# Performance work log

Measured on AMD Instinct MI355X. Metric: run time of the kernel, lower is better.

## Reference

```python
import math
import jax, jax.numpy as jnp
import numpy as np

# ---- static config ----
B, S, HID = 2, 8192, 1024
H, D = 8, 128                      # num_heads, head_dim = hidden // heads
CHUNK = 128                        # attention_chunk_size
PAST = 128 - 1                     # attention_context_left - 1
FUT = 128                          # attention_context_right
CTX = CHUNK + PAST + FUT           # 383
POS = CTX + 1                      # relative position table length (rel_shift pads to CTX+1)
CAP = 50.0                         # attention_logit_cap
Q_SCALE = D ** (-0.5) / math.log(2.0)
K_SCALE = math.log1p(math.e) / math.log(2.0)
NB = S // CHUNK                    # 64 blocks (S divisible by chunk -> no tail padding)


def setup_inputs() -> dict:
    key = jax.random.key(0)
    ks = jax.random.split(key, 8)
    s = 0.02
    return {
        "hidden_states": jax.random.normal(ks[0], (B, S, HID), jnp.float32),
        "position_embeddings": jax.random.normal(ks[1], (POS, HID), jnp.float32),
        "Wq": jax.random.normal(ks[2], (HID, H * D), jnp.float32) * s,
        "Wk": jax.random.normal(ks[3], (HID, H * D), jnp.float32) * s,
        "Wv": jax.random.normal(ks[4], (HID, H * D), jnp.float32) * s,
        "Wrel": jax.random.normal(ks[5], (HID, H * D), jnp.float32) * s,
        "Wpost": jax.random.normal(ks[6], (HID, HID), jnp.float32) * s,
        "per_dim_scale": jax.random.normal(ks[7], (D,), jnp.float32) * 0.1,
    }


def reference(hidden_states, position_embeddings, Wq, Wk, Wv, Wrel, Wpost, per_dim_scale):
    # projections (clipped-linear clamps are +/-inf -> no-ops); bias-free linears
    q = (hidden_states @ Wq).reshape(B, S, H, D)
    k = (hidden_states @ Wk).reshape(B, S, H, D)
    v = (hidden_states @ Wv).reshape(B, S, H, D)

    q = q * (Q_SCALE * jax.nn.softplus(per_dim_scale))  # per-dim scaling fused into q
    k = k * K_SCALE

    # _convert_to_block: [B, NB, CHUNK, H, D] (S % CHUNK == 0 -> no pad)
    qb = q.reshape(B, NB, CHUNK, H, D)

    # _extract_block_context: pad (PAST, FUT + CHUNK - 1) then unfold window=CTX step=CHUNK
    pad = ((0, 0), (PAST, FUT + CHUNK - 1), (0, 0), (0, 0))
    kp = jnp.pad(k, pad)
    vp = jnp.pad(v, pad)
    idx = jnp.arange(NB)[:, None] * CHUNK + jnp.arange(CTX)[None, :]  # [NB, CTX]
    kc = kp[:, idx]  # [B, NB, CTX, H, D]
    vc = vp[:, idx]  # [B, NB, CTX, H, D]

    # relative keys: [POS, H, D]
    rel_k = (position_embeddings @ Wrel).reshape(POS, H, D)

    # content scores: [B, H, NB, CHUNK, CTX]
    ac = jnp.einsum('bnchd,bnkhd->bhnck', qb, kc)
    # position scores before shift: [B, H, NB, CHUNK, POS]
    bd = jnp.einsum('bnchd,phd->bhncp', qb, rel_k)
    # Transformer-XL rel_shift (POS == CTX+1 so pad amount is zero)
    bd = bd.reshape(B, H, NB, CHUNK * POS)[..., : CHUNK * CTX]
    bd = bd.reshape(B, H, NB, CHUNK, CTX)

    # tanh soft-cap + softmax (no attention_mask)
    logits = jnp.tanh((ac + bd) / CAP) * CAP
    attn = jax.nn.softmax(logits, axis=-1)

    # weighted values -> [B, NB, CHUNK, H, D] -> [B, S, HID]
    out = jnp.einsum('bhnck,bnkhd->bnchd', attn, vc).reshape(B, S, H * D)
    return out @ Wpost
```

## Files before the change

### kernel.cpp

```cpp
#include <hip/hip_runtime.h>
#include <cmath>


using bf16x8 = __attribute__((ext_vector_type(8))) short;
using f32x4  = __attribute__((ext_vector_type(4))) float;
using s16x4  = __attribute__((ext_vector_type(4))) short;

__device__ __forceinline__ short f2bf(float f) {
  unsigned u = __float_as_uint(f);
  u = (u + 0x7FFF + ((u >> 16) & 1)) >> 16;
  return (short)u;
}
__device__ __forceinline__ float bf2f(unsigned short s) {
  return __uint_as_float(((unsigned)s) << 16);
}

__device__ __forceinline__ void gl16(void* lds, const void* gptr) {
  __builtin_amdgcn_global_load_lds(
      (const __attribute__((address_space(1))) unsigned int*)gptr,
      (__attribute__((address_space(3))) unsigned int*)lds, 16, 0, 0);
}

__global__ void cvt_bf16_k(const float* __restrict__ in, short* __restrict__ out, int n) {
  int i = (blockIdx.x * 256 + threadIdx.x) * 4;
  if (i + 3 < n) {
    float4 v = *(const float4*)&in[i];
    s16x4 o;
    o[0] = f2bf(v.x); o[1] = f2bf(v.y); o[2] = f2bf(v.z); o[3] = f2bf(v.w);
    *(s16x4*)&out[i] = o;
  }
}

__global__ void wtrans_k(const float* __restrict__ W, short* __restrict__ Wt) {
  __shared__ float T[64 * 65];
  const int tid = threadIdx.x;
  const int bx = blockIdx.x, by = blockIdx.y;
#pragma unroll
  for (int it = 0; it < 4; ++it) {
    int ci = it * 256 + tid;
    int k = ci >> 4, n4 = (ci & 15) * 4;
    float4 v = *(const float4*)&W[(size_t)(by * 64 + k) * 1024 + bx * 64 + n4];
    T[k * 65 + n4 + 0] = v.x;
    T[k * 65 + n4 + 1] = v.y;
    T[k * 65 + n4 + 2] = v.z;
    T[k * 65 + n4 + 3] = v.w;
  }
  __syncthreads();
#pragma unroll
  for (int it = 0; it < 2; ++it) {
    int co = it * 256 + tid;
    int nn = co >> 3, k8 = (co & 7) * 8;
    bf16x8 o;
#pragma unroll
    for (int jj = 0; jj < 8; ++jj) o[jj] = f2bf(T[(k8 + jj) * 65 + nn]);
    *(bf16x8*)&Wt[(size_t)(bx * 64 + nn) * 1024 + by * 64 + k8] = o;
  }
}

__global__ void qscale_k(const float* __restrict__ pds, float* __restrict__ qs, double qsb) {
  int d = threadIdx.x;
  double x = (double)pds[d];
  qs[d] = (float)(qsb * log1p(exp(x)));
}

__global__ void vpadzero_k(short* __restrict__ vpadT) {
  int row = blockIdx.x;
  int t = threadIdx.x;
  int key = (t < 127) ? t : (8192 + t);
  vpadT[(size_t)row * 8448 + key] = 0;
}


__device__ __forceinline__ void stage_half(short* ldsb, const short* gbase, int tid) {
#pragma unroll
  for (int it = 0; it < 2; ++it) {
    int L = (it * 512 + tid) * 16;
    int r = L >> 7;
    int cb = (L & 127) ^ (((L >> 9) & 1) << 5);
    gl16((char*)ldsb + L, gbase + (size_t)r * 1024 + (cb >> 1));
  }
}

__device__ __forceinline__ bf16x8 frag_ld(const short* hb, int row, int ks, int q4) {
  int cb = (ks * 64 + q4 * 16) ^ (((row >> 2) & 1) << 5);
  return *(const bf16x8*)((const char*)hb + row * 128 + cb);
}

__global__ __launch_bounds__(512, 2)
void qkv256_k(const short* __restrict__ A, const short* __restrict__ Bt3,
              short* __restrict__ q_bf, short* __restrict__ kpad,
              short* __restrict__ vpadT,
              const float* __restrict__ qsc, float kscale) {
  __shared__ __align__(16) short lds[65536];

  const int tid = threadIdx.x;
  const int lane = tid & 63, wid = tid >> 6;
  const int q4 = lane >> 4, l16 = lane & 15;
  const int wr = wid >> 2, wc = wid & 3;

  const int id = blockIdx.x;
  const int xcd = id & 7, local = id >> 3;
  const int mm = xcd * 8 + local / 12, nn = local % 12;
  const int m0 = mm * 256, n0 = nn * 256;

  const short* Abase = A + (size_t)m0 * 1024;
  const short* Bbase = Bt3 + (size_t)n0 * 1024;

  const f32x4 z4 = {0.f, 0.f, 0.f, 0.f};
  f32x4 acc[8][4];
#pragma unroll
  for (int i = 0; i < 8; ++i)
#pragma unroll
    for (int j = 0; j < 4; ++j) acc[i][j] = z4;

  stage_half(lds + 0 * 32768 + 0 * 8192, Abase, tid);
  stage_half(lds + 0 * 32768 + 1 * 8192, Abase + 128 * 1024, tid);
  stage_half(lds + 0 * 32768 + 2 * 8192, Bbase, tid);
  stage_half(lds + 0 * 32768 + 3 * 8192, Bbase + 128 * 1024, tid);
  stage_half(lds + 1 * 32768 + 2 * 8192, Bbase + 64, tid);
  stage_half(lds + 1 * 32768 + 3 * 8192, Bbase + 128 * 1024 + 64, tid);
  asm volatile("s_waitcnt vmcnt(4)" ::: "memory");
  __builtin_amdgcn_s_barrier();

  for (int kt = 0; kt < 16; ++kt) {
    const int buf = kt & 1;
    const short* Acur = lds + buf * 32768 + wr * 8192;
    const short* Bcur = lds + buf * 32768 + (2 + (wc >> 1)) * 8192;
    const int brow0 = (wc & 1) * 64;

    bf16x8 bfr[4][2];

    {
#pragma unroll
      for (int j = 0; j < 4; ++j)
#pragma unroll
        for (int ks = 0; ks < 2; ++ks)
          bfr[j][ks] = frag_ld(Bcur, brow0 + j * 16 + l16, ks, q4);
      bf16x8 afr[2][2];
#pragma unroll
      for (int m2 = 0; m2 < 2; ++m2)
#pragma unroll
        for (int ks = 0; ks < 2; ++ks)
          afr[m2][ks] = frag_ld(Acur, m2 * 16 + l16, ks, q4);
      if (kt < 15)
        stage_half(lds + (buf ^ 1) * 32768 + 0 * 8192, Abase + (size_t)(kt + 1) * 64, tid);
      asm volatile("s_waitcnt lgkmcnt(8)" ::: "memory");
      __builtin_amdgcn_s_barrier();
      asm volatile("s_waitcnt lgkmcnt(0)" ::: "memory");
      __builtin_amdgcn_s_setprio(1);
#pragma unroll
      for (int ks = 0; ks < 2; ++ks)
#pragma unroll
        for (int m2 = 0; m2 < 2; ++m2)
#pragma unroll
          for (int j = 0; j < 4; ++j)
            acc[m2][j] = __builtin_amdgcn_mfma_f32_16x16x32_bf16(
                afr[m2][ks], bfr[j][ks], acc[m2][j], 0, 0, 0);
      __builtin_amdgcn_s_setprio(0);
      __builtin_amdgcn_s_barrier();
    }

#pragma unroll
    for (int p = 1; p < 4; ++p) {
      bf16x8 afr[2][2];
#pragma unroll
      for (int m2 = 0; m2 < 2; ++m2)
#pragma unroll
        for (int ks = 0; ks < 2; ++ks)
          afr[m2][ks] = frag_ld(Acur, (p * 2 + m2) * 16 + l16, ks, q4);
      if (p == 1) {
        if (kt < 15)
          stage_half(lds + (buf ^ 1) * 32768 + 1 * 8192,
                     Abase + 128 * 1024 + (size_t)(kt + 1) * 64, tid);
      } else if (p == 2) {
        if (kt < 14)
          stage_half(lds + buf * 32768 + 2 * 8192, Bbase + (size_t)(kt + 2) * 64, tid);
      } else {
        if (kt < 14)
          stage_half(lds + buf * 32768 + 3 * 8192,
                     Bbase + 128 * 1024 + (size_t)(kt + 2) * 64, tid);
      }
      __builtin_amdgcn_s_barrier();
      asm volatile("s_waitcnt lgkmcnt(0)" ::: "memory");
      __builtin_amdgcn_s_setprio(1);
#pragma unroll
      for (int ks = 0; ks < 2; ++ks)
#pragma unroll
        for (int m2 = 0; m2 < 2; ++m2)
#pragma unroll
          for (int j = 0; j < 4; ++j)
            acc[p * 2 + m2][j] = __builtin_amdgcn_mfma_f32_16x16x32_bf16(
                afr[m2][ks], bfr[j][ks], acc[p * 2 + m2][j], 0, 0, 0);
      __builtin_amdgcn_s_setprio(0);
      if (p == 3) {
        if (kt < 14) asm volatile("s_waitcnt vmcnt(4)" ::: "memory");
        else         asm volatile("s_waitcnt vmcnt(0)" ::: "memory");
      }
      __builtin_amdgcn_s_barrier();
    }
  }

  const int w = n0 >> 10;
  const int cw = n0 & 1023;
  const int b = m0 >> 13;
  const int s_base = (m0 & 8191) + wr * 128;

  if (w == 0) {
    float qsv[4];
#pragma unroll
    for (int j = 0; j < 4; ++j) qsv[j] = qsc[(cw + wc * 64 + j * 16 + l16) & 127];
#pragma unroll
    for (int m = 0; m < 8; ++m)
#pragma unroll
      for (int j = 0; j < 4; ++j)
#pragma unroll
        for (int rg = 0; rg < 4; ++rg) {
          int s = s_base + m * 16 + q4 * 4 + rg;
          int col = cw + wc * 64 + j * 16 + l16;
          int h = col >> 7, d = col & 127;
          int n = s >> 7, c = s & 127;
          q_bf[((size_t)(((b * 64 + n) * 8 + h) * 128 + c)) * 128 + d] =
              f2bf(acc[m][j][rg] * qsv[j]);
        }
  } else if (w == 1) {
#pragma unroll
    for (int m = 0; m < 8; ++m)
#pragma unroll
      for (int j = 0; j < 4; ++j)
#pragma unroll
        for (int rg = 0; rg < 4; ++rg) {
          int s = s_base + m * 16 + q4 * 4 + rg;
          int col = cw + wc * 64 + j * 16 + l16;
          int h = col >> 7, d = col & 127;
          kpad[((size_t)(b * 8 + h) * 8448 + 127 + s) * 128 + d] =
              f2bf(acc[m][j][rg] * kscale);
        }
  } else {
    short* T = lds;
#pragma unroll
    for (int hh = 0; hh < 2; ++hh) {
      __syncthreads();
      if ((wc >> 1) == hh) {
#pragma unroll
        for (int m = 0; m < 8; ++m)
#pragma unroll
          for (int j = 0; j < 4; ++j)
#pragma unroll
            for (int rg = 0; rg < 4; ++rg) {
              int sl = wr * 128 + m * 16 + q4 * 4 + rg;
              int dl = (wc & 1) * 64 + j * 16 + l16;
              T[dl * 264 + sl] = f2bf(acc[m][j][rg]);
            }
      }
      __syncthreads();
      const int h = (cw >> 7) + hh;
#pragma unroll
      for (int it = 0; it < 8; ++it) {
        int co = it * 512 + tid;
        int dd = co >> 5, s8 = (co & 31) * 8;
        *(bf16x8*)&vpadT[((size_t)(b * 8 + h) * 128 + dd) * 8448 + 127 + (m0 & 8191) + s8] =
            *(const bf16x8*)&T[dd * 264 + s8];
      }
    }
  }
}

__global__ __launch_bounds__(256, 3)
void post_gemm_k(const short* __restrict__ A, const short* __restrict__ Bt,
                 float* __restrict__ outf) {
  __shared__ __align__(16) short As[128 * 32];
  __shared__ __align__(16) short Bs[128 * 32];

  const int tid = threadIdx.x;
  const int lane = tid & 63, wid = tid >> 6;
  const int q4 = lane >> 4, l16 = lane & 15;
  const int wr = wid >> 1, wc = wid & 1;

  const int id = blockIdx.x;
  const int xcd = id & 7, local = id >> 3;
  const int mm = local >> 3, nn = local & 7;
  const int m0 = (xcd * 16 + mm) * 128, n0 = nn * 128;

  const f32x4 z4 = {0.f, 0.f, 0.f, 0.f};
  f32x4 acc[4][4];
#pragma unroll
  for (int i = 0; i < 4; ++i)
#pragma unroll
    for (int j = 0; j < 4; ++j) acc[i][j] = z4;

  const int r0 = tid >> 2, s0_ = (tid & 3) * 8;

  for (int kk = 0; kk < 1024; kk += 32) {
    __syncthreads();
    gl16(&As[tid * 8],         A  + (size_t)(m0 + r0) * 1024 + kk + s0_);
    gl16(&Bs[tid * 8],         Bt + (size_t)(n0 + r0) * 1024 + kk + s0_);
    gl16(&As[(256 + tid) * 8], A  + (size_t)(m0 + 64 + r0) * 1024 + kk + s0_);
    gl16(&Bs[(256 + tid) * 8], Bt + (size_t)(n0 + 64 + r0) * 1024 + kk + s0_);
    __syncthreads();
    bf16x8 af[4], bfv[4];
#pragma unroll
    for (int i = 0; i < 4; ++i)
      af[i] = *(const bf16x8*)&As[(wr * 64 + i * 16 + l16) * 32 + q4 * 8];
#pragma unroll
    for (int j = 0; j < 4; ++j)
      bfv[j] = *(const bf16x8*)&Bs[(wc * 64 + j * 16 + l16) * 32 + q4 * 8];
#pragma unroll
    for (int i = 0; i < 4; ++i)
#pragma unroll
      for (int j = 0; j < 4; ++j)
        acc[i][j] = __builtin_amdgcn_mfma_f32_16x16x32_bf16(af[i], bfv[j], acc[i][j], 0, 0, 0);
  }

#pragma unroll
  for (int i = 0; i < 4; ++i)
#pragma unroll
    for (int j = 0; j < 4; ++j)
#pragma unroll
      for (int rg = 0; rg < 4; ++rg) {
        const int row = m0 + wr * 64 + i * 16 + q4 * 4 + rg;
        const int col = n0 + wc * 64 + j * 16 + l16;
        outf[(size_t)row * 1024 + col] = acc[i][j][rg];
      }
}

__global__ __launch_bounds__(256, 2)
void rel_gemm_k(const short* __restrict__ A, const short* __restrict__ Bt,
                short* __restrict__ relk) {
  __shared__ __align__(16) short As[128 * 32];
  __shared__ __align__(16) short Bs[128 * 32];

  const int tid = threadIdx.x;
  const int lane = tid & 63, wid = tid >> 6;
  const int q4 = lane >> 4, l16 = lane & 15;
  const int wr = wid >> 1, wc = wid & 1;
  const int m0 = blockIdx.x * 128, n0 = blockIdx.y * 128;

  const f32x4 z4 = {0.f, 0.f, 0.f, 0.f};
  f32x4 acc[4][4];
#pragma unroll
  for (int i = 0; i < 4; ++i)
#pragma unroll
    for (int j = 0; j < 4; ++j) acc[i][j] = z4;

  const int r0 = tid >> 2, s0_ = (tid & 3) * 8;
  for (int kk = 0; kk < 1024; kk += 32) {
    __syncthreads();
    gl16(&As[tid * 8],         A  + (size_t)(m0 + r0) * 1024 + kk + s0_);
    gl16(&Bs[tid * 8],         Bt + (size_t)(n0 + r0) * 1024 + kk + s0_);
    gl16(&As[(256 + tid) * 8], A  + (size_t)(m0 + 64 + r0) * 1024 + kk + s0_);
    gl16(&Bs[(256 + tid) * 8], Bt + (size_t)(n0 + 64 + r0) * 1024 + kk + s0_);
    __syncthreads();
    bf16x8 af[4], bfv[4];
#pragma unroll
    for (int i = 0; i < 4; ++i)
      af[i] = *(const bf16x8*)&As[(wr * 64 + i * 16 + l16) * 32 + q4 * 8];
#pragma unroll
    for (int j = 0; j < 4; ++j)
      bfv[j] = *(const bf16x8*)&Bs[(wc * 64 + j * 16 + l16) * 32 + q4 * 8];
#pragma unroll
    for (int i = 0; i < 4; ++i)
#pragma unroll
      for (int j = 0; j < 4; ++j)
        acc[i][j] = __builtin_amdgcn_mfma_f32_16x16x32_bf16(af[i], bfv[j], acc[i][j], 0, 0, 0);
  }

#pragma unroll
  for (int i = 0; i < 4; ++i)
#pragma unroll
    for (int j = 0; j < 4; ++j)
#pragma unroll
      for (int rg = 0; rg < 4; ++rg) {
        const int row = m0 + wr * 64 + i * 16 + q4 * 4 + rg;
        const int col = n0 + wc * 64 + j * 16 + l16;
        int h = col >> 7, d = col & 127;
        relk[(size_t)(h * 384 + row) * 128 + d] = f2bf(acc[i][j][rg]);
      }
}

__global__ __launch_bounds__(256, 2)
void bd_gemm_k(const short* __restrict__ qb_b, const short* __restrict__ relk,
               short* __restrict__ bds) {
  __shared__ __align__(16) short As[128 * 32];
  __shared__ __align__(16) short Bs[128 * 32];
  const int tid = threadIdx.x;
  const int lane = tid & 63, wid = tid >> 6;
  const int q4 = lane >> 4, l16 = lane & 15;
  const int wr = wid >> 1, wc = wid & 1;
  const int p0 = blockIdx.x * 128;
  const int nh = blockIdx.y;
  const int h = nh & 7;
  const short* A = qb_b + (size_t)nh * 16384;
  const short* Bt = relk + (size_t)h * (384 * 128);
  short* bdo = bds + (size_t)nh * 49152;

  const f32x4 z4 = {0.f, 0.f, 0.f, 0.f};
  f32x4 acc[4][4];
#pragma unroll
  for (int i = 0; i < 4; ++i)
#pragma unroll
    for (int j = 0; j < 4; ++j) acc[i][j] = z4;

  const int r0 = tid >> 2, s0_ = (tid & 3) * 8;
  for (int kk = 0; kk < 128; kk += 32) {
    __syncthreads();
    gl16(&As[tid * 8],         A  + (size_t)r0 * 128 + kk + s0_);
    gl16(&Bs[tid * 8],         Bt + (size_t)(p0 + r0) * 128 + kk + s0_);
    gl16(&As[(256 + tid) * 8], A  + (size_t)(64 + r0) * 128 + kk + s0_);
    gl16(&Bs[(256 + tid) * 8], Bt + (size_t)(p0 + 64 + r0) * 128 + kk + s0_);
    __syncthreads();
    bf16x8 af[4], bfv[4];
#pragma unroll
    for (int i = 0; i < 4; ++i)
      af[i] = *(const bf16x8*)&As[(wr * 64 + i * 16 + l16) * 32 + q4 * 8];
#pragma unroll
    for (int j = 0; j < 4; ++j)
      bfv[j] = *(const bf16x8*)&Bs[(wc * 64 + j * 16 + l16) * 32 + q4 * 8];
#pragma unroll
    for (int i = 0; i < 4; ++i)
#pragma unroll
      for (int j = 0; j < 4; ++j)
        acc[i][j] = __builtin_amdgcn_mfma_f32_16x16x32_bf16(af[i], bfv[j], acc[i][j], 0, 0, 0);
  }

#pragma unroll
  for (int i = 0; i < 4; ++i)
#pragma unroll
    for (int j = 0; j < 4; ++j)
#pragma unroll
      for (int rg = 0; rg < 4; ++rg) {
        int r = wr * 64 + i * 16 + q4 * 4 + rg;
        int p = p0 + wc * 64 + j * 16 + l16;
        int t = r + p;
        int c = (t < 383) ? r : (r + 1);
        int k = (t < 383) ? t : (t - 383);
        if (c < 128) {
          int tt = k >> 7, jj = (k >> 4) & 7, ll = k & 15;
          int wa = c >> 5, ia = (c >> 4) & 1, qa = (c >> 2) & 3, ra = c & 3;
          bdo[((((size_t)tt * 8 + jj) * 256) + wa * 64 + qa * 16 + ll) * 8 + ia * 4 + ra] =
              f2bf(acc[i][j][rg]);
        }
      }
}

__global__ __launch_bounds__(256, 3)
void attn_k(const short* __restrict__ qb_b, const short* __restrict__ kpad,
            const short* __restrict__ vpadT, const short* __restrict__ bds,
            short* __restrict__ attnout, int b) {
  __shared__ __align__(16) short Ks[4 * 128 * 32];
  __shared__ __align__(16) short Ps[64 * 136];

  const int tid = threadIdx.x;
  const int lane = tid & 63, wid = tid >> 6;
  const int q4 = lane >> 4, l16 = lane & 15;
  const int bx = blockIdx.x;
  const int qh = bx & 1, nh = bx >> 1;
  const int n = nh >> 3, h = nh & 7;

  const short* qtile = qb_b + (size_t)nh * 16384 + qh * 64 * 128;
  const short* kbase = kpad + ((size_t)(b * 8 + h) * 8448 + n * 128) * 128;
  const short* vtb = vpadT + (size_t)(b * 8 + h) * 128 * 8448 + n * 128;
  const short* bdb = bds + (size_t)nh * 49152;

#pragma unroll
  for (int it = 0; it < 4; ++it) {
    int ci = it * 256 + tid;
    int dc = ci >> 8, rr = (ci >> 2) & 63, sub = (ci & 3) * 8;
    gl16(&Ks[ci * 8], qtile + rr * 128 + dc * 32 + sub);
  }
  __syncthreads();
  bf16x8 qf[4];
#pragma unroll
  for (int dc = 0; dc < 4; ++dc)
    qf[dc] = *(const bf16x8*)&Ks[dc * 2048 + (wid * 16 + l16) * 32 + q4 * 8];

  const f32x4 z4 = {0.f, 0.f, 0.f, 0.f};
  f32x4 acco[8];
#pragma unroll
  for (int j = 0; j < 8; ++j) acco[j] = z4;
  float rsum[4] = {};

  for (int t = 0; t < 3; ++t) {
    __syncthreads();
#pragma unroll
    for (int it = 0; it < 8; ++it) {
      int ci = it * 256 + tid;
      int dc = ci >> 9, rr = (ci >> 2) & 127, sub = (ci & 3) * 8;
      gl16(&Ks[ci * 8], kbase + (size_t)(t * 128 + rr) * 128 + dc * 32 + sub);
    }

    s16x4 bdv[8];
#pragma unroll
    for (int j = 0; j < 8; ++j)
      bdv[j] = *(const s16x4*)&bdb[((((size_t)t * 8 + j) * 256) +
                 (qh * 2 + (wid >> 1)) * 64 + q4 * 16 + l16) * 8 + (wid & 1) * 4];

    __syncthreads();

    f32x4 accs[8];
#pragma unroll
    for (int j = 0; j < 8; ++j) accs[j] = z4;
#pragma unroll
    for (int dc = 0; dc < 4; ++dc) {
      bf16x8 kf[8];
#pragma unroll
      for (int j = 0; j < 8; ++j)
        kf[j] = *(const bf16x8*)&Ks[dc * 4096 + (j * 16 + l16) * 32 + q4 * 8];
#pragma unroll
      for (int j = 0; j < 8; ++j)
        accs[j] = __builtin_amdgcn_mfma_f32_16x16x32_bf16(qf[dc], kf[j], accs[j], 0, 0, 0);
    }

#pragma unroll
    for (int j = 0; j < 8; ++j) {
      const int kg = t * 128 + j * 16 + l16;
#pragma unroll
      for (int rg = 0; rg < 4; ++rg) {
        float sv = accs[j][rg] + bf2f((unsigned short)bdv[j][rg]);
        float tt = exp2f(sv * 0.057707801635558534f);
        float wgt = exp2f(-144.26950408889634f * __fdividef(1.0f, tt + 1.0f));
        wgt = (kg < 383) ? wgt : 0.0f;
        accs[j][rg] = wgt;
        rsum[rg] += wgt;
      }
    }
    __syncthreads();

#pragma unroll
    for (int it = 0; it < 8; ++it) {
      int ci = it * 256 + tid;
      int kc = ci >> 9, dd = (ci >> 2) & 127, sub = (ci & 3) * 8;
      gl16(&Ks[ci * 8], vtb + (size_t)dd * 8448 + t * 128 + kc * 32 + sub);
    }
#pragma unroll
    for (int j = 0; j < 8; ++j)
#pragma unroll
      for (int rg = 0; rg < 4; ++rg) {
        int c = wid * 16 + q4 * 4 + rg;
        int kl = j * 16 + l16;
        Ps[c * 136 + kl] = f2bf(accs[j][rg]);
      }
    __syncthreads();

#pragma unroll
    for (int kc = 0; kc < 4; ++kc) {
      bf16x8 pf, vf[8];
      pf = *(const bf16x8*)&Ps[(wid * 16 + l16) * 136 + kc * 32 + q4 * 8];
#pragma unroll
      for (int j = 0; j < 8; ++j)
        vf[j] = *(const bf16x8*)&Ks[kc * 4096 + (j * 16 + l16) * 32 + q4 * 8];
#pragma unroll
      for (int j = 0; j < 8; ++j)
        acco[j] = __builtin_amdgcn_mfma_f32_16x16x32_bf16(pf, vf[j], acco[j], 0, 0, 0);
    }
  }

  float rinv[4];
#pragma unroll
  for (int rg = 0; rg < 4; ++rg) {
    float rs = rsum[rg];
    rs += __shfl_xor(rs, 1);
    rs += __shfl_xor(rs, 2);
    rs += __shfl_xor(rs, 4);
    rs += __shfl_xor(rs, 8);
    rinv[rg] = __fdividef(1.0f, rs);
  }
#pragma unroll
  for (int j = 0; j < 8; ++j)
#pragma unroll
    for (int rg = 0; rg < 4; ++rg) {
      int srow = n * 128 + qh * 64 + wid * 16 + q4 * 4 + rg;
      int col = h * 128 + j * 16 + l16;
      attnout[((size_t)b * 8192 + srow) * 1024 + col] = f2bf(acco[j][rg] * rinv[rg]);
    }
}

extern "C" void kernel_launch(void* const* d_in, const int* in_sizes, int n_in,
                              void* d_out, int out_size, void* d_ws, size_t ws_size,
                              hipStream_t stream) {
  (void)in_sizes; (void)n_in; (void)out_size; (void)ws_size;
  const float* hs    = (const float*)d_in[0];
  const float* pemb  = (const float*)d_in[1];
  const float* Wq    = (const float*)d_in[2];
  const float* Wk    = (const float*)d_in[3];
  const float* Wv    = (const float*)d_in[4];
  const float* Wrel  = (const float*)d_in[5];
  const float* Wpost = (const float*)d_in[6];
  const float* pds   = (const float*)d_in[7];
  float* out = (float*)d_out;

  char* w = (char*)d_ws;
  auto alloc = [&](size_t bytes) -> char* {
    char* p = w; w += (bytes + 255) & ~(size_t)255; return p;
  };
  short* hs_bf   = (short*)alloc((size_t)16384 * 1024 * 2);
  short* pos_bf  = (short*)alloc((size_t)384 * 1024 * 2);
  short* Wq_t    = (short*)alloc((size_t)1024 * 1024 * 2);
  short* Wk_t    = (short*)alloc((size_t)1024 * 1024 * 2);
  short* Wv_t    = (short*)alloc((size_t)1024 * 1024 * 2);
  short* Wrel_t  = (short*)alloc((size_t)1024 * 1024 * 2);
  short* Wpost_t = (short*)alloc((size_t)1024 * 1024 * 2);
  float* qsc     = (float*)alloc(512);
  short* q_bf    = (short*)alloc((size_t)2 * 64 * 8 * 128 * 128 * 2);
  short* kpad    = (short*)alloc((size_t)2 * 8 * 8448 * 128 * 2);
  short* vpadT   = (short*)alloc((size_t)2 * 8 * 128 * 8448 * 2);
  short* relk    = (short*)alloc((size_t)8 * 384 * 128 * 2);
  short* bds     = (short*)alloc((size_t)64 * 8 * 128 * 384 * 2);
  short* attnout = hs_bf;

  const float kscale = (float)(log1p(exp(1.0)) / log(2.0));
  const double qsb = (1.0 / sqrt(128.0)) / log(2.0);

  cvt_bf16_k<<<16384, 256, 0, stream>>>(hs, hs_bf, 16384 * 1024);
  cvt_bf16_k<<<384, 256, 0, stream>>>(pemb, pos_bf, 384 * 1024);
  dim3 tg(16, 16);
  wtrans_k<<<tg, 256, 0, stream>>>(Wq, Wq_t);
  wtrans_k<<<tg, 256, 0, stream>>>(Wk, Wk_t);
  wtrans_k<<<tg, 256, 0, stream>>>(Wv, Wv_t);
  wtrans_k<<<tg, 256, 0, stream>>>(Wrel, Wrel_t);
  wtrans_k<<<tg, 256, 0, stream>>>(Wpost, Wpost_t);
  qscale_k<<<1, 128, 0, stream>>>(pds, qsc, qsb);
  hipMemsetAsync(kpad, 0, (size_t)2 * 8 * 8448 * 128 * 2, stream);
  vpadzero_k<<<2048, 256, 0, stream>>>(vpadT);

  qkv256_k<<<768, 512, 0, stream>>>(hs_bf, Wq_t, q_bf, kpad, vpadT, qsc, kscale);
  rel_gemm_k<<<dim3(3, 8), 256, 0, stream>>>(pos_bf, Wrel_t, relk);

  for (int b = 0; b < 2; ++b) {
    const short* qb_b = q_bf + (size_t)b * 64 * 8 * 128 * 128;
    bd_gemm_k<<<dim3(3, 512), 256, 0, stream>>>(qb_b, relk, bds);
    attn_k<<<1024, 256, 0, stream>>>(qb_b, kpad, vpadT, bds, attnout, b);
  }

  post_gemm_k<<<1024, 256, 0, stream>>>(attnout, Wpost_t, out);
}
```

Measured before the change: 544.2 us.

## Replace post-projection GEMM with 256x256 double-buffered pipelined kernel and XOR swizzle

The output projection GEMM moves from 128x128 tiles with a single 32-wide K stage to 256x256 tiles with 512 threads, 64-wide K steps, double-buffered LDS, staggered async global-to-LDS loads and MFMA priority hints. This is the same scheme the QKV kernel uses. The LDS swizzle is changed to a full 8-slot XOR pattern that both the QKV and post kernels share, to reduce bank conflicts. It cuts per-tile load overhead and barrier stalls, but launches only 256 blocks and relies on hand-placed waitcnt and barriers being correct.

```diff
diff --git a/kernel.cpp b/kernel.cpp
--- a/kernel.cpp
+++ b/kernel.cpp
@@ -74,16 +74,17 @@
 __device__ __forceinline__ void stage_half(short* ldsb, const short* gbase, int tid) {
 #pragma unroll
   for (int it = 0; it < 2; ++it) {
-    int L = (it * 512 + tid) * 16;
-    int r = L >> 7;
-    int cb = (L & 127) ^ (((L >> 9) & 1) << 5);
-    gl16((char*)ldsb + L, gbase + (size_t)r * 1024 + (cb >> 1));
+    int idx = it * 512 + tid;
+    int r = idx >> 3;
+    int slot = idx & 7;
+    int src = (slot ^ (r & 7)) << 3;
+    gl16((char*)ldsb + idx * 16, gbase + (size_t)r * 1024 + src);
   }
 }
 
 __device__ __forceinline__ bf16x8 frag_ld(const short* hb, int row, int ks, int q4) {
-  int cb = (ks * 64 + q4 * 16) ^ (((row >> 2) & 1) << 5);
-  return *(const bf16x8*)((const char*)hb + row * 128 + cb);
+  int slot = (ks * 4 + q4) ^ (row & 7);
+  return *(const bf16x8*)((const char*)hb + row * 128 + slot * 16);
 }
 
 __global__ __launch_bounds__(512, 2)
@@ -265,61 +266,127 @@
   }
 }
 
-__global__ __launch_bounds__(256, 3)
-void post_gemm_k(const short* __restrict__ A, const short* __restrict__ Bt,
-                 float* __restrict__ outf) {
-  __shared__ __align__(16) short As[128 * 32];
-  __shared__ __align__(16) short Bs[128 * 32];
+__global__ __launch_bounds__(512, 2)
+void post256_k(const short* __restrict__ A, const short* __restrict__ Bt,
+               float* __restrict__ outf) {
+  __shared__ __align__(16) short lds[65536];
 
   const int tid = threadIdx.x;
   const int lane = tid & 63, wid = tid >> 6;
   const int q4 = lane >> 4, l16 = lane & 15;
-  const int wr = wid >> 1, wc = wid & 1;
+  const int wr = wid >> 2, wc = wid & 3;
 
   const int id = blockIdx.x;
   const int xcd = id & 7, local = id >> 3;
-  const int mm = local >> 3, nn = local & 7;
-  const int m0 = (xcd * 16 + mm) * 128, n0 = nn * 128;
+  const int mm = xcd * 8 + (local >> 2), nn = local & 3;
+  const int m0 = mm * 256, n0 = nn * 256;
+
+  const short* Abase = A + (size_t)m0 * 1024;
+  const short* Bbase = Bt + (size_t)n0 * 1024;
 
   const f32x4 z4 = {0.f, 0.f, 0.f, 0.f};
-  f32x4 acc[4][4];
-#pragma unroll
-  for (int i = 0; i < 4; ++i)
+  f32x4 acc[8][4];
+#pragma unroll
+  for (int i = 0; i < 8; ++i)
 #pragma unroll
     for (int j = 0; j < 4; ++j) acc[i][j] = z4;
 
-  const int r0 = tid >> 2, s0_ = (tid & 3) * 8;
-
-  for (int kk = 0; kk < 1024; kk += 32) {
-    __syncthreads();
-    gl16(&As[tid * 8],         A  + (size_t)(m0 + r0) * 1024 + kk + s0_);
-    gl16(&Bs[tid * 8],         Bt + (size_t)(n0 + r0) * 1024 + kk + s0_);
-    gl16(&As[(256 + tid) * 8], A  + (size_t)(m0 + 64 + r0) * 1024 + kk + s0_);
-    gl16(&Bs[(256 + tid) * 8], Bt + (size_t)(n0 + 64 + r0) * 1024 + kk + s0_);
-    __syncthreads();
-    bf16x8 af[4], bfv[4];
-#pragma unroll
-    for (int i = 0; i < 4; ++i)
-      af[i] = *(const bf16x8*)&As[(wr * 64 + i * 16 + l16) * 32 + q4 * 8];
+  stage_half(lds + 0 * 32768 + 0 * 8192, Abase, tid);
+  stage_half(lds + 0 * 32768 + 1 * 8192, Abase + 128 * 1024, tid);
+  stage_half(lds + 0 * 32768 + 2 * 8192, Bbase, tid);
+  stage_half(lds + 0 * 32768 + 3 * 8192, Bbase + 128 * 1024, tid);
+  stage_half(lds + 1 * 32768 + 2 * 8192, Bbase + 64, tid);
+  stage_half(lds + 1 * 32768 + 3 * 8192, Bbase + 128 * 1024 + 64, tid);
+  asm volatile("s_waitcnt vmcnt(4)" ::: "memory");
+  __builtin_amdgcn_s_barrier();
+
+  for (int kt = 0; kt < 16; ++kt) {
+    const int buf = kt & 1;
+    const short* Acur = lds + buf * 32768 + wr * 8192;
+    const short* Bcur = lds + buf * 32768 + (2 + (wc >> 1)) * 8192;
+    const int brow0 = (wc & 1) * 64;
+
+    bf16x8 bfr[4][2];
+
+    {
+#pragma unroll
+      for (int j = 0; j < 4; ++j)
+#pragma unroll
+        for (int ks = 0; ks < 2; ++ks)
+          bfr[j][ks] = frag_ld(Bcur, brow0 + j * 16 + l16, ks, q4);
+      bf16x8 afr[2][2];
+#pragma unroll
+      for (int m2 = 0; m2 < 2; ++m2)
+#pragma unroll
+        for (int ks = 0; ks < 2; ++ks)
+          afr[m2][ks] = frag_ld(Acur, m2 * 16 + l16, ks, q4);
+      if (kt < 15)
+        stage_half(lds + (buf ^ 1) * 32768 + 0 * 8192, Abase + (size_t)(kt + 1) * 64, tid);
+      asm volatile("s_waitcnt lgkmcnt(8)" ::: "memory");
+      __builtin_amdgcn_s_barrier();
+      asm volatile("s_waitcnt lgkmcnt(0)" ::: "memory");
+      __builtin_amdgcn_s_setprio(1);
+#pragma unroll
+      for (int ks = 0; ks < 2; ++ks)
+#pragma unroll
+        for (int m2 = 0; m2 < 2; ++m2)
+#pragma unroll
+          for (int j = 0; j < 4; ++j)
+            acc[m2][j] = __builtin_amdgcn_mfma_f32_16x16x32_bf16(
+                afr[m2][ks], bfr[j][ks], acc[m2][j], 0, 0, 0);
+      __builtin_amdgcn_s_setprio(0);
+      __builtin_amdgcn_s_barrier();
+    }
+
+#pragma unroll
+    for (int p = 1; p < 4; ++p) {
+      bf16x8 afr[2][2];
+#pragma unroll
+      for (int m2 = 0; m2 < 2; ++m2)
+#pragma unroll
+        for (int ks = 0; ks < 2; ++ks)
+          afr[m2][ks] = frag_ld(Acur, (p * 2 + m2) * 16 + l16, ks, q4);
+      if (p == 1) {
+        if (kt < 15)
+          stage_half(lds + (buf ^ 1) * 32768 + 1 * 8192,
+                     Abase + 128 * 1024 + (size_t)(kt + 1) * 64, tid);
+      } else if (p == 2) {
+        if (kt < 14)
+          stage_half(lds + buf * 32768 + 2 * 8192, Bbase + (size_t)(kt + 2) * 64, tid);
+      } else {
+        if (kt < 14)
+          stage_half(lds + buf * 32768 + 3 * 8192,
+                     Bbase + 128 * 1024 + (size_t)(kt + 2) * 64, tid);
+      }
+      __builtin_amdgcn_s_barrier();
+      asm volatile("s_waitcnt lgkmcnt(0)" ::: "memory");
+      __builtin_amdgcn_s_setprio(1);
+#pragma unroll
+      for (int ks = 0; ks < 2; ++ks)
+#pragma unroll
+        for (int m2 = 0; m2 < 2; ++m2)
+#pragma unroll
+          for (int j = 0; j < 4; ++j)
+            acc[p * 2 + m2][j] = __builtin_amdgcn_mfma_f32_16x16x32_bf16(
+                afr[m2][ks], bfr[j][ks], acc[p * 2 + m2][j], 0, 0, 0);
+      __builtin_amdgcn_s_setprio(0);
+      if (p == 3) {
+        if (kt < 14) asm volatile("s_waitcnt vmcnt(4)" ::: "memory");
+        else         asm volatile("s_waitcnt vmcnt(0)" ::: "memory");
+      }
+      __builtin_amdgcn_s_barrier();
+    }
+  }
+
+#pragma unroll
+  for (int m = 0; m < 8; ++m)
 #pragma unroll
     for (int j = 0; j < 4; ++j)
-      bfv[j] = *(const bf16x8*)&Bs[(wc * 64 + j * 16 + l16) * 32 + q4 * 8];
-#pragma unroll
-    for (int i = 0; i < 4; ++i)
-#pragma unroll
-      for (int j = 0; j < 4; ++j)
-        acc[i][j] = __builtin_amdgcn_mfma_f32_16x16x32_bf16(af[i], bfv[j], acc[i][j], 0, 0, 0);
-  }
-
-#pragma unroll
-  for (int i = 0; i < 4; ++i)
-#pragma unroll
-    for (int j = 0; j < 4; ++j)
 #pragma unroll
       for (int rg = 0; rg < 4; ++rg) {
-        const int row = m0 + wr * 64 + i * 16 + q4 * 4 + rg;
+        const int row = m0 + wr * 128 + m * 16 + q4 * 4 + rg;
         const int col = n0 + wc * 64 + j * 16 + l16;
-        outf[(size_t)row * 1024 + col] = acc[i][j][rg];
+        outf[(size_t)row * 1024 + col] = acc[m][j][rg];
       }
 }
 
@@ -631,5 +698,5 @@
     attn_k<<<1024, 256, 0, stream>>>(qb_b, kpad, vpadT, bds, attnout, b);
   }
 
-  post_gemm_k<<<1024, 256, 0, stream>>>(attnout, Wpost_t, out);
-}
+  post256_k<<<256, 512, 0, stream>>>(attnout, Wpost_t, out);
+}
```

Result: faster. 505.2 us (-7.2%).
